# Kernel optimization log

Measured on AMD Instinct MI355X. Metric: run time of the kernel, lower is better.

Reference implementation:

```python
import jax, jax.numpy as jnp
import numpy as np


def _update_cv(features, labels, ave, cov, amount, class_num):
    # Segment-reduce formulation of the onehot-expand update_CV.
    N, A = features.shape
    C = class_num
    counts = jax.ops.segment_sum(jnp.ones((N,), features.dtype), labels, num_segments=C)  # [C]
    sums = jax.ops.segment_sum(features, labels, num_segments=C)  # [C, A]
    denom = jnp.where(counts == 0, 1.0, counts)[:, None]  # Amount_CxA with zeros -> 1
    ave_CxA = sums / denom
    # var_temp: sum over samples of (x - mean_label)^2, divided by count
    diff = features - ave_CxA[labels]  # [N, A]
    sq = jax.ops.segment_sum(diff * diff, labels, num_segments=C)
    var_temp = sq / denom
    sum_weight = counts[:, None]  # [C,1] broadcast over A
    weight_CV = sum_weight / (sum_weight + amount[:, None])
    weight_CV = jnp.nan_to_num(weight_CV, nan=0.0)
    additional_CV = weight_CV * (1 - weight_CV) * (ave - ave_CxA) ** 2
    new_cov = cov * (1 - weight_CV) + var_temp * weight_CV + additional_CV
    new_ave = ave * (1 - weight_CV) + ave_CxA * weight_CV
    new_amount = amount + counts
    return new_ave, new_cov, new_amount


def _isda_aug(fc_weight, y, labels, cv_matrix, ratio):
    # sigma2[n,c] = ratio * sum_a (W[c,a] - W[labels[n],a])^2 * CV[labels[n],a]
    # = ratio * ( (W^2) @ cv_n - 2 W @ (w_n * cv_n) + sum_a w_n^2 cv_n )
    cv_n = cv_matrix[labels]              # [N, A]
    w_n = fc_weight[labels]               # [N, A]
    t1 = cv_n @ (fc_weight ** 2).T        # [N, C]
    t2 = (w_n * cv_n) @ fc_weight.T       # [N, C]
    t3 = jnp.sum(w_n * w_n * cv_n, axis=1, keepdims=True)  # [N, 1]
    sigma2 = ratio * (t1 - 2.0 * t2 + t3)
    return y + 0.5 * sigma2


def setup_inputs() -> dict:
    key = jax.random.key(0)
    k1, k2, k3, k4 = jax.random.split(key, 4)
    N, A, C = 512, 2048, 1000
    features = jax.random.normal(k1, (N, A), dtype=jnp.float32)
    labels = jax.random.randint(k2, (N,), 0, C)
    fc_weight = jax.random.normal(k3, (C, A), dtype=jnp.float32) * 0.02
    fc_bias = jax.random.normal(k4, (C,), dtype=jnp.float32) * 0.02
    return {
        "features": features,
        "labels": labels,
        "fc_weight": fc_weight,
        "fc_bias": fc_bias,
        "ave_state": jnp.zeros((C, A), jnp.float32),
        "cov_state": jnp.zeros((C, A), jnp.float32),
        "amount_state": jnp.zeros((C,), jnp.float32),
        "ratio": 1,
    }


def reference(features, labels, fc_weight, fc_bias, ave_state, cov_state, amount_state, ratio):
    C = fc_weight.shape[0]
    # model head: y = features @ W^T + b (features come from backbone; detached for CV)
    y = features @ fc_weight.T + fc_bias
    new_ave, new_cov, new_amount = _update_cv(
        jax.lax.stop_gradient(features), labels, ave_state, cov_state, amount_state, C)
    isda_y = _isda_aug(fc_weight, y, labels, jax.lax.stop_gradient(new_cov), ratio)
    log_probs = jax.nn.log_softmax(isda_y, axis=1)
    loss = -jnp.mean(jnp.take_along_axis(log_probs, labels[:, None], axis=1))
    return loss, y, new_ave, new_cov, new_amount
```

## Files before the change

### kernel.cpp

```cpp
#include <hip/hip_runtime.h>
#include <hip/hip_bf16.h>

typedef short v8s __attribute__((ext_vector_type(8)));
typedef float v4f __attribute__((ext_vector_type(4)));

#define KSPLIT 4

static __device__ __forceinline__ float ldv(const void* p, size_t i, int f32m) {
    if (f32m) return ((const float*)p)[i];
    return __bfloat162float(((const __hip_bfloat16*)p)[i]);
}
static __device__ __forceinline__ void stv(void* p, size_t i, float v, int f32m) {
    if (f32m) ((float*)p)[i] = v;
    else ((__hip_bfloat16*)p)[i] = __float2bfloat16(v);
}
static __device__ __forceinline__ unsigned short f2bu(float x) {
    __hip_bfloat16 h = __float2bfloat16(x);
    return *(unsigned short*)&h;
}
static __device__ __forceinline__ float bu2f(unsigned short u) {
    return __uint_as_float(((unsigned)u) << 16);
}

static __device__ __forceinline__ float decode_scalar(const void* p) {
    unsigned u = *(const unsigned*)p;
    unsigned e32 = (u >> 23) & 0xff;
    if (e32 >= 97 && e32 <= 160) return __uint_as_float(u);
    unsigned lo = u & 0xffffu;
    unsigned e16 = (lo >> 7) & 0xff;
    if ((u >> 16) == 0 && e16 >= 97 && e16 <= 160)
        return __uint_as_float(lo << 16);
    return (float)(int)u;
}

static __device__ __forceinline__ int block_sniff(const void* feat) {
    const __hip_bfloat16* p = (const __hip_bfloat16*)feat;
    float v = __bfloat162float(p[threadIdx.x & 255]);
    int bad = !(fabsf(v) < 1e10f);
    return __syncthreads_or(bad) ? 1 : 0;
}

__device__ __forceinline__ float wave_sum(float v) {
    #pragma unroll
    for (int o = 32; o > 0; o >>= 1) v += __shfl_down(v, o, 64);
    return v;
}
__device__ __forceinline__ float wave_max(float v) {
    #pragma unroll
    for (int o = 32; o > 0; o >>= 1) v = fmaxf(v, __shfl_down(v, o, 64));
    return v;
}

__global__ __launch_bounds__(256) void prep_sort(
        const void* __restrict__ feat, unsigned short* __restrict__ featb, int total,
        const int* __restrict__ labels, int* __restrict__ counts,
        int* __restrict__ offs, int* __restrict__ rows,
        float* __restrict__ misc, int Nn, int C) {
    int f32m = block_sniff(feat);
    int tid = threadIdx.x;
    int i = (blockIdx.x * 256 + tid) * 8;
    if (i < total) {
        if (f32m) {
            const float* f = (const float*)feat + i;
            unsigned short r[8];
            #pragma unroll
            for (int u = 0; u < 8; ++u) r[u] = f2bu(f[u]);
            *(v8s*)(featb + i) = *(v8s*)r;
        } else {
            *(v8s*)(featb + i) = *(const v8s*)((const unsigned short*)feat + i);
        }
    }
    if (blockIdx.x != 0) return;

    if (tid < 16) misc[tid] = 0.f;

    __shared__ int h[1024];
    __shared__ int ex[256];
    __shared__ int cur[1024];
    #pragma unroll
    for (int u = 0; u < 4; ++u) h[tid + 256 * u] = 0;
    __syncthreads();
    for (int k = tid; k < Nn; k += 256) atomicAdd(&h[labels[k]], 1);
    __syncthreads();
    int b0 = h[4 * tid], b1 = h[4 * tid + 1], b2 = h[4 * tid + 2], b3 = h[4 * tid + 3];
    int s = b0 + b1 + b2 + b3;
    ex[tid] = s;
    __syncthreads();
    for (int d = 1; d < 256; d <<= 1) {
        int v = (tid >= d) ? ex[tid - d] : 0;
        __syncthreads();
        ex[tid] += v;
        __syncthreads();
    }
    int excl = ex[tid] - s;
    int o0 = excl, o1 = o0 + b0, o2 = o1 + b1, o3 = o2 + b2;
    counts[4 * tid] = b0; counts[4 * tid + 1] = b1;
    counts[4 * tid + 2] = b2; counts[4 * tid + 3] = b3;
    offs[4 * tid] = o0; offs[4 * tid + 1] = o1;
    offs[4 * tid + 2] = o2; offs[4 * tid + 3] = o3;
    cur[4 * tid] = o0; cur[4 * tid + 1] = o1;
    cur[4 * tid + 2] = o2; cur[4 * tid + 3] = o3;
    __syncthreads();
    for (int k = tid; k < Nn; k += 256) {
        int pos = atomicAdd(&cur[labels[k]], 1);
        rows[pos] = k;
    }
}

__global__ __launch_bounds__(256) void finalize_stats(
        const unsigned short* __restrict__ featb,
        const int* __restrict__ counts, const int* __restrict__ offs,
        const int* __restrict__ rows,
        const void* __restrict__ ave, const void* __restrict__ cov,
        const void* __restrict__ amount, const void* __restrict__ W,
        const void* __restrict__ feat,
        void* __restrict__ out, size_t off_ave, size_t off_cov, size_t off_amt,
        unsigned short* __restrict__ Wb, unsigned short* __restrict__ W2b,
        unsigned short* __restrict__ Cb, unsigned short* __restrict__ Gb,
        float* __restrict__ T3p, int A, int A8) {
    __shared__ float sb[4];
    int f32m = block_sniff(feat);
    int c = blockIdx.y;
    int a = blockIdx.x * 256 + threadIdx.x;
    size_t idx = (size_t)c * A + a;
    int cnti = counts[c];
    int start = offs[c];
    float s1 = 0.f, s2 = 0.f;
    for (int i = 0; i < cnti; ++i) {
        float x = bu2f(featb[(size_t)rows[start + i] * A + a]);
        s1 += x;
        s2 += x * x;
    }
    float cnt = (float)cnti;
    float denom = cnti > 0 ? cnt : 1.f;
    float mean = s1 / denom;
    float var = fmaxf((s2 - cnt * mean * mean) / denom, 0.f);
    float amt = ldv(amount, c, f32m);
    float tot = cnt + amt;
    float w = tot > 0.f ? (cnt / tot) : 0.f;
    float av = ldv(ave, idx, f32m);
    float cv = ldv(cov, idx, f32m);
    float d = av - mean;
    float ncv = cv * (1.f - w) + var * w + w * (1.f - w) * d * d;
    float nav = av * (1.f - w) + mean * w;
    stv(out, off_cov + idx, ncv, f32m);
    stv(out, off_ave + idx, nav, f32m);
    float wv = ldv(W, idx, f32m);
    Wb[idx] = f2bu(wv);
    W2b[idx] = f2bu(wv * wv);
    Cb[idx] = f2bu(ncv);
    Gb[idx] = f2bu(ncv * wv);
    if (a == 0) stv(out, off_amt + c, amt + cnt, f32m);
    float s = wave_sum(wv * wv * ncv);
    int lane = threadIdx.x & 63, wid = threadIdx.x >> 6;
    if (lane == 0) sb[wid] = s;
    __syncthreads();
    if (threadIdx.x == 0) T3p[(size_t)c * A8 + blockIdx.x] = sb[0] + sb[1] + sb[2] + sb[3];
}

__global__ __launch_bounds__(256) void triple_gemm_mfma(
        const unsigned short* __restrict__ featb,
        const unsigned short* __restrict__ Wb,
        const unsigned short* __restrict__ W2b,
        const unsigned short* __restrict__ Cb,
        const unsigned short* __restrict__ Gb,
        const int* __restrict__ labels,
        float* __restrict__ partY, float* __restrict__ partT1, float* __restrict__ partT2,
        int Cpad, int A, size_t NC) {
    int tid = threadIdx.x, wv = tid >> 6, lane = tid & 63;
    int n0 = blockIdx.y * 64, j0 = blockIdx.x * 64;
    int kslice = A / KSPLIT;
    int k0 = blockIdx.z * kslice;
    int r = lane & 15, q = lane >> 4;

    int nrow = n0 + wv * 16 + r;
    int lab = labels[nrow];
    const unsigned short* pF = featb + (size_t)nrow * A + k0 + q * 8;
    const unsigned short* pC = Cb + (size_t)lab * A + k0 + q * 8;
    const unsigned short* pG = Gb + (size_t)lab * A + k0 + q * 8;
    const unsigned short* pW0 = Wb  + (size_t)(j0 + 0  + r) * A + k0 + q * 8;
    const unsigned short* pW1 = Wb  + (size_t)(j0 + 16 + r) * A + k0 + q * 8;
    const unsigned short* pW2 = Wb  + (size_t)(j0 + 32 + r) * A + k0 + q * 8;
    const unsigned short* pW3 = Wb  + (size_t)(j0 + 48 + r) * A + k0 + q * 8;
    const unsigned short* pQ0 = W2b + (size_t)(j0 + 0  + r) * A + k0 + q * 8;
    const unsigned short* pQ1 = W2b + (size_t)(j0 + 16 + r) * A + k0 + q * 8;
    const unsigned short* pQ2 = W2b + (size_t)(j0 + 32 + r) * A + k0 + q * 8;
    const unsigned short* pQ3 = W2b + (size_t)(j0 + 48 + r) * A + k0 + q * 8;

    v4f aY[4] = {{0,0,0,0},{0,0,0,0},{0,0,0,0},{0,0,0,0}};
    v4f aT1[4] = {{0,0,0,0},{0,0,0,0},{0,0,0,0},{0,0,0,0}};
    v4f aT2[4] = {{0,0,0,0},{0,0,0,0},{0,0,0,0},{0,0,0,0}};

    for (int kk = 0; kk < kslice; kk += 32) {
        v8s f = *(const v8s*)pF;
        v8s c = *(const v8s*)pC;
        v8s g = *(const v8s*)pG;
        v8s w0 = *(const v8s*)pW0, w1 = *(const v8s*)pW1;
        v8s w2 = *(const v8s*)pW2, w3 = *(const v8s*)pW3;
        v8s q0 = *(const v8s*)pQ0, q1 = *(const v8s*)pQ1;
        v8s q2 = *(const v8s*)pQ2, q3 = *(const v8s*)pQ3;
        pF += 32; pC += 32; pG += 32;
        pW0 += 32; pW1 += 32; pW2 += 32; pW3 += 32;
        pQ0 += 32; pQ1 += 32; pQ2 += 32; pQ3 += 32;

        aY[0]  = __builtin_amdgcn_mfma_f32_16x16x32_bf16(f, w0, aY[0],  0, 0, 0);
        aY[1]  = __builtin_amdgcn_mfma_f32_16x16x32_bf16(f, w1, aY[1],  0, 0, 0);
        aY[2]  = __builtin_amdgcn_mfma_f32_16x16x32_bf16(f, w2, aY[2],  0, 0, 0);
        aY[3]  = __builtin_amdgcn_mfma_f32_16x16x32_bf16(f, w3, aY[3],  0, 0, 0);
        aT1[0] = __builtin_amdgcn_mfma_f32_16x16x32_bf16(c, q0, aT1[0], 0, 0, 0);
        aT1[1] = __builtin_amdgcn_mfma_f32_16x16x32_bf16(c, q1, aT1[1], 0, 0, 0);
        aT1[2] = __builtin_amdgcn_mfma_f32_16x16x32_bf16(c, q2, aT1[2], 0, 0, 0);
        aT1[3] = __builtin_amdgcn_mfma_f32_16x16x32_bf16(c, q3, aT1[3], 0, 0, 0);
        aT2[0] = __builtin_amdgcn_mfma_f32_16x16x32_bf16(g, w0, aT2[0], 0, 0, 0);
        aT2[1] = __builtin_amdgcn_mfma_f32_16x16x32_bf16(g, w1, aT2[1], 0, 0, 0);
        aT2[2] = __builtin_amdgcn_mfma_f32_16x16x32_bf16(g, w2, aT2[2], 0, 0, 0);
        aT2[3] = __builtin_amdgcn_mfma_f32_16x16x32_bf16(g, w3, aT2[3], 0, 0, 0);
    }

    float* pY = partY + (size_t)blockIdx.z * NC;
    float* p1 = partT1 + (size_t)blockIdx.z * NC;
    float* p2 = partT2 + (size_t)blockIdx.z * NC;
    int quad = lane >> 4, colb = lane & 15;
    #pragma unroll
    for (int t = 0; t < 4; ++t) {
        int j = j0 + t * 16 + colb;
        #pragma unroll
        for (int rr = 0; rr < 4; ++rr) {
            int n = n0 + wv * 16 + quad * 4 + rr;
            size_t idx = (size_t)n * Cpad + j;
            pY[idx] = aY[t][rr];
            p1[idx] = aT1[t][rr];
            p2[idx] = aT2[t][rr];
        }
    }
}

__global__ __launch_bounds__(256) void epilogue_rowloss(
        const float* __restrict__ partY, const float* __restrict__ partT1,
        const float* __restrict__ partT2, const float* __restrict__ T3p,
        const void* __restrict__ bias, const void* __restrict__ feat,
        const int* __restrict__ labels,
        void* __restrict__ out, size_t off_y,
        float* __restrict__ misc,
        int C, int Cpad, int A8, const void* ratio_p, size_t NC, int Nn) {
    __shared__ float sb[4];
    __shared__ float sM;
    __shared__ float sLabVal;
    int f32m = block_sniff(feat);
    int tid = threadIdx.x;
    int n = blockIdx.x;
    int lab = labels[n];
    float t3 = 0.f;
    for (int i = 0; i < A8; ++i) t3 += T3p[(size_t)lab * A8 + i];
    float ratio = decode_scalar(ratio_p);

    float vals[8];
    int nu = Cpad >> 8;
    float m = -3.4e38f;
    for (int u = 0; u < nu; ++u) {
        int j = u * 256 + tid;
        float v = -3.4e38f;
        if (j < C) {
            size_t idx = (size_t)n * Cpad + j;
            float y = 0.f, t1 = 0.f, t2 = 0.f;
            #pragma unroll
            for (int z = 0; z < KSPLIT; ++z) {
                y  += partY[z * NC + idx];
                t1 += partT1[z * NC + idx];
                t2 += partT2[z * NC + idx];
            }
            y += ldv(bias, j, f32m);
            stv(out, off_y + (size_t)n * C + j, y, f32m);
            v = y + 0.5f * ratio * (t1 - 2.f * t2 + t3);
            if (j == lab) sLabVal = v;
        }
        vals[u] = v;
        m = fmaxf(m, v);
    }
    m = wave_max(m);
    int lane = tid & 63, wid = tid >> 6;
    if (lane == 0) sb[wid] = m;
    __syncthreads();
    if (tid == 0) sM = fmaxf(fmaxf(sb[0], sb[1]), fmaxf(sb[2], sb[3]));
    __syncthreads();
    m = sM;
    float s = 0.f;
    for (int u = 0; u < nu; ++u) s += expf(vals[u] - m);
    __syncthreads();
    s = wave_sum(s);
    if (lane == 0) sb[wid] = s;
    __syncthreads();
    if (tid == 0) {
        float rl = m + logf(sb[0] + sb[1] + sb[2] + sb[3]) - sLabVal;
        atomicAdd(&misc[0], rl);
        __threadfence();
        int old = atomicAdd((int*)&misc[1], 1);
        if (old == Nn - 1) {
            __threadfence();
            float tot = atomicAdd(&misc[0], 0.f);
            stv(out, 0, tot / (float)Nn, f32m);
        }
    }
}

extern "C" void kernel_launch(void* const* d_in, const int* in_sizes, int n_in,
                              void* d_out, int out_size, void* d_ws, size_t ws_size,
                              hipStream_t stream) {
    const void* feat   = d_in[0];
    const int*  labels = (const int*)d_in[1];
    const void* W      = d_in[2];
    const void* bias   = d_in[3];
    const void* ave    = d_in[4];
    const void* cov    = d_in[5];
    const void* amount = d_in[6];
    const void* ratiop = d_in[7];

    int NA = in_sizes[0];
    int Nn = in_sizes[1];
    int C  = in_sizes[3];
    int A  = NA / Nn;
    int CA = in_sizes[2];
    int Cpad = ((C + 255) / 256) * 256;
    int A8 = A / 256;
    size_t NC = (size_t)Nn * Cpad;

    size_t off_y   = 1;
    size_t off_ave = off_y + (size_t)Nn * C;
    size_t off_cov = off_ave + (size_t)CA;
    size_t off_amt = off_cov + (size_t)CA;

    char* ws = (char*)d_ws;
    int*   w_cnt  = (int*)ws;
    int*   w_off  = w_cnt + 1024;
    int*   w_rows = w_off + 1024;
    float* w_misc = (float*)(w_rows + 1024);
    float* w_T3p  = w_misc + 16;
    float* w_partY  = w_T3p + 8192;
    float* w_partT1 = w_partY + KSPLIT * NC;
    float* w_partT2 = w_partT1 + KSPLIT * NC;
    unsigned short* w_featb = (unsigned short*)(w_partT2 + KSPLIT * NC);
    unsigned short* w_Wb    = w_featb + NA;
    unsigned short* w_W2b   = w_Wb + CA;
    unsigned short* w_Cb    = w_W2b + CA;
    unsigned short* w_Gb    = w_Cb + CA;

    prep_sort<<<NA / 2048, 256, 0, stream>>>(feat, w_featb, NA, labels,
                                             w_cnt, w_off, w_rows, w_misc, Nn, C);
    dim3 g2(A8, C);
    finalize_stats<<<g2, 256, 0, stream>>>(w_featb, w_cnt, w_off, w_rows,
                                           ave, cov, amount, W, feat,
                                           d_out, off_ave, off_cov, off_amt,
                                           w_Wb, w_W2b, w_Cb, w_Gb, w_T3p, A, A8);
    dim3 g3(Cpad / 64, Nn / 64, KSPLIT);
    triple_gemm_mfma<<<g3, 256, 0, stream>>>(w_featb, w_Wb, w_W2b, w_Cb, w_Gb,
                                             labels, w_partY, w_partT1, w_partT2,
                                             Cpad, A, NC);
    epilogue_rowloss<<<Nn, 256, 0, stream>>>(w_partY, w_partT1, w_partT2, w_T3p,
                                             bias, feat, labels, d_out, off_y,
                                             w_misc, C, Cpad, A8, ratiop, NC, Nn);
}
```

Measured before the change: 164.7 us.

## Stage GEMM operands through LDS via direct global-to-LDS loads

The triple GEMM kernel stops having each wave load all four W and W2 row tiles straight from global memory. Each wave now loads only its own 16-row slice of every operand into shared memory with global_load_lds, and the waves then share the W/W2 tiles from LDS. The K step per iteration doubles to 64. This cuts redundant global loads of the weight tiles by about 4x, at the cost of two block-wide barriers per iteration and no double buffering, so load latency is not overlapped with the MFMAs.

```diff
diff --git a/kernel.cpp b/kernel.cpp
--- a/kernel.cpp
+++ b/kernel.cpp
@@ -49,6 +49,13 @@
     #pragma unroll
     for (int o = 32; o > 0; o >>= 1) v = fmaxf(v, __shfl_down(v, o, 64));
     return v;
+}
+
+static __device__ __forceinline__ void ld16(unsigned short* lds, const unsigned short* g) {
+    __builtin_amdgcn_global_load_lds(
+        (const __attribute__((address_space(1))) unsigned int*)g,
+        (__attribute__((address_space(3))) unsigned int*)lds,
+        16, 0, 0);
 }
 
 __global__ __launch_bounds__(256) void prep_sort(
@@ -167,54 +174,56 @@
         const int* __restrict__ labels,
         float* __restrict__ partY, float* __restrict__ partT1, float* __restrict__ partT2,
         int Cpad, int A, size_t NC) {
+    __shared__ unsigned short sA[20480];
+    __shared__ int sLab[64];
     int tid = threadIdx.x, wv = tid >> 6, lane = tid & 63;
     int n0 = blockIdx.y * 64, j0 = blockIdx.x * 64;
     int kslice = A / KSPLIT;
     int k0 = blockIdx.z * kslice;
+    if (tid < 64) sLab[tid] = labels[n0 + tid];
+    __syncthreads();
+
     int r = lane & 15, q = lane >> 4;
-
-    int nrow = n0 + wv * 16 + r;
-    int lab = labels[nrow];
-    const unsigned short* pF = featb + (size_t)nrow * A + k0 + q * 8;
+    int fr = wv * 16 + r;
+    const unsigned short* pF = featb + (size_t)(n0 + fr) * A + k0 + q * 8;
+    int lab = sLab[fr];
     const unsigned short* pC = Cb + (size_t)lab * A + k0 + q * 8;
     const unsigned short* pG = Gb + (size_t)lab * A + k0 + q * 8;
-    const unsigned short* pW0 = Wb  + (size_t)(j0 + 0  + r) * A + k0 + q * 8;
-    const unsigned short* pW1 = Wb  + (size_t)(j0 + 16 + r) * A + k0 + q * 8;
-    const unsigned short* pW2 = Wb  + (size_t)(j0 + 32 + r) * A + k0 + q * 8;
-    const unsigned short* pW3 = Wb  + (size_t)(j0 + 48 + r) * A + k0 + q * 8;
-    const unsigned short* pQ0 = W2b + (size_t)(j0 + 0  + r) * A + k0 + q * 8;
-    const unsigned short* pQ1 = W2b + (size_t)(j0 + 16 + r) * A + k0 + q * 8;
-    const unsigned short* pQ2 = W2b + (size_t)(j0 + 32 + r) * A + k0 + q * 8;
-    const unsigned short* pQ3 = W2b + (size_t)(j0 + 48 + r) * A + k0 + q * 8;
+    const unsigned short* pW = Wb  + (size_t)(j0 + fr) * A + k0 + q * 8;
+    const unsigned short* pQ = W2b + (size_t)(j0 + fr) * A + k0 + q * 8;
+    unsigned short* dF = &sA[0     + wv * 1024];
+    unsigned short* dC = &sA[4096  + wv * 1024];
+    unsigned short* dG = &sA[8192  + wv * 1024];
+    unsigned short* dW = &sA[12288 + wv * 1024];
+    unsigned short* dQ = &sA[16384 + wv * 1024];
 
     v4f aY[4] = {{0,0,0,0},{0,0,0,0},{0,0,0,0},{0,0,0,0}};
     v4f aT1[4] = {{0,0,0,0},{0,0,0,0},{0,0,0,0},{0,0,0,0}};
     v4f aT2[4] = {{0,0,0,0},{0,0,0,0},{0,0,0,0},{0,0,0,0}};
 
-    for (int kk = 0; kk < kslice; kk += 32) {
-        v8s f = *(const v8s*)pF;
-        v8s c = *(const v8s*)pC;
-        v8s g = *(const v8s*)pG;
-        v8s w0 = *(const v8s*)pW0, w1 = *(const v8s*)pW1;
-        v8s w2 = *(const v8s*)pW2, w3 = *(const v8s*)pW3;
-        v8s q0 = *(const v8s*)pQ0, q1 = *(const v8s*)pQ1;
-        v8s q2 = *(const v8s*)pQ2, q3 = *(const v8s*)pQ3;
-        pF += 32; pC += 32; pG += 32;
-        pW0 += 32; pW1 += 32; pW2 += 32; pW3 += 32;
-        pQ0 += 32; pQ1 += 32; pQ2 += 32; pQ3 += 32;
-
-        aY[0]  = __builtin_amdgcn_mfma_f32_16x16x32_bf16(f, w0, aY[0],  0, 0, 0);
-        aY[1]  = __builtin_amdgcn_mfma_f32_16x16x32_bf16(f, w1, aY[1],  0, 0, 0);
-        aY[2]  = __builtin_amdgcn_mfma_f32_16x16x32_bf16(f, w2, aY[2],  0, 0, 0);
-        aY[3]  = __builtin_amdgcn_mfma_f32_16x16x32_bf16(f, w3, aY[3],  0, 0, 0);
-        aT1[0] = __builtin_amdgcn_mfma_f32_16x16x32_bf16(c, q0, aT1[0], 0, 0, 0);
-        aT1[1] = __builtin_amdgcn_mfma_f32_16x16x32_bf16(c, q1, aT1[1], 0, 0, 0);
-        aT1[2] = __builtin_amdgcn_mfma_f32_16x16x32_bf16(c, q2, aT1[2], 0, 0, 0);
-        aT1[3] = __builtin_amdgcn_mfma_f32_16x16x32_bf16(c, q3, aT1[3], 0, 0, 0);
-        aT2[0] = __builtin_amdgcn_mfma_f32_16x16x32_bf16(g, w0, aT2[0], 0, 0, 0);
-        aT2[1] = __builtin_amdgcn_mfma_f32_16x16x32_bf16(g, w1, aT2[1], 0, 0, 0);
-        aT2[2] = __builtin_amdgcn_mfma_f32_16x16x32_bf16(g, w2, aT2[2], 0, 0, 0);
-        aT2[3] = __builtin_amdgcn_mfma_f32_16x16x32_bf16(g, w3, aT2[3], 0, 0, 0);
+    for (int kk = 0; kk < kslice; kk += 64) {
+        ld16(dF, pF); ld16(dF + 512, pF + 32);
+        ld16(dC, pC); ld16(dC + 512, pC + 32);
+        ld16(dG, pG); ld16(dG + 512, pG + 32);
+        ld16(dW, pW); ld16(dW + 512, pW + 32);
+        ld16(dQ, pQ); ld16(dQ + 512, pQ + 32);
+        pF += 64; pC += 64; pG += 64; pW += 64; pQ += 64;
+        __syncthreads();
+        #pragma unroll
+        for (int s = 0; s < 2; ++s) {
+            v8s f = *(v8s*)&sA[0    + wv * 1024 + s * 512 + lane * 8];
+            v8s c = *(v8s*)&sA[4096 + wv * 1024 + s * 512 + lane * 8];
+            v8s g = *(v8s*)&sA[8192 + wv * 1024 + s * 512 + lane * 8];
+            #pragma unroll
+            for (int t = 0; t < 4; ++t) {
+                v8s w  = *(v8s*)&sA[12288 + t * 1024 + s * 512 + lane * 8];
+                v8s w2 = *(v8s*)&sA[16384 + t * 1024 + s * 512 + lane * 8];
+                aY[t]  = __builtin_amdgcn_mfma_f32_16x16x32_bf16(f, w,  aY[t],  0, 0, 0);
+                aT1[t] = __builtin_amdgcn_mfma_f32_16x16x32_bf16(c, w2, aT1[t], 0, 0, 0);
+                aT2[t] = __builtin_amdgcn_mfma_f32_16x16x32_bf16(g, w,  aT2[t], 0, 0, 0);
+            }
+        }
+        __syncthreads();
     }
 
     float* pY = partY + (size_t)blockIdx.z * NC;
```

New measurement: 146.7 us. -10.9%, faster.
